# Optimization experiments

Measured on AMD Instinct MI355X. Metric: run time of the kernel, lower is better.

## Reference

```python
import jax, jax.numpy as jnp
import numpy as np
import itertools, math

DIM = 3          # Cl(3,0), Euclidean metric (1,1,1)
N_BLADES = 2 ** DIM   # 8
N_GRADES = DIM + 1    # 4 subspaces with sizes [1,3,3,1]
EPS = 1e-6

def _build_algebra():
    # blades ordered by grade then lexicographic, matching CEGNN's CliffordAlgebra
    blades = [()] + [c for g in range(1, DIM + 1) for c in itertools.combinations(range(DIM), g)]
    masks = [sum(1 << i for i in b) for b in blades]
    idx = {m: i for i, m in enumerate(masks)}
    grades = np.array([bin(m).count('1') for m in masks])

    def sign(a, b):  # reordering sign for e_A * e_B (Euclidean: squares are +1)
        s, aa = 0, a >> 1
        while aa:
            s += bin(aa & b).count('1')
            aa >>= 1
        return (-1.0) ** s

    cayley = np.zeros((N_BLADES, N_BLADES, N_BLADES), np.float32)
    for i, mi in enumerate(masks):
        for k, mk in enumerate(masks):
            cayley[i, idx[mi ^ mk], k] = sign(mi, mk)  # out_j = x_i C[i,j,k] y_k

    paths = np.zeros((N_GRADES, N_GRADES, N_GRADES), bool)
    for gi in range(N_GRADES):
        for gj in range(N_GRADES):
            for gk in range(N_GRADES):
                paths[gi, gj, gk] = np.any(cayley[np.ix_(grades == gi, grades == gj, grades == gk)] != 0)
    return cayley, grades, paths

CAYLEY, GRADES, PATHS = _build_algebra()
PATH_IDX = np.argwhere(PATHS)                                  # [20, 3]
GRADE_IDX = [np.nonzero(GRADES == g)[0] for g in range(N_GRADES)]
N_PATHS = int(PATHS.sum())                                     # 20 for Cl(3,0)

B, F = 8192, 256


def setup_inputs() -> dict:
    key = jax.random.key(0)
    ks = jax.random.split(key, 4)
    std_lin = 1.0 / math.sqrt(F)
    x = jax.random.normal(ks[0], (B, F, N_BLADES), jnp.float32)
    w_left = jax.random.normal(ks[1], (F, F, N_GRADES), jnp.float32) * std_lin
    b_left = jnp.zeros((1, F, 1), jnp.float32)
    w_right = jax.random.normal(ks[2], (F, F, N_GRADES), jnp.float32) * std_lin
    a_norm = jnp.zeros((F, N_GRADES), jnp.float32)
    w_gp = jax.random.normal(ks[3], (F, N_PATHS), jnp.float32) * (1.0 / math.sqrt(DIM + 1))
    return {"x": x, "w_left": w_left, "b_left": b_left, "w_right": w_right,
            "a_norm": a_norm, "w_gp": w_gp}


def _mv_linear(x, w):
    # w: [n, m, n_grades] -> repeat_interleave by grade sizes via gather to [n, m, 8]
    return jnp.einsum('bmi,nmi->bni', x, w[:, :, GRADES])


def _normalize(xr, a_norm):
    # per-grade smooth-abs-sqrt norm: (q^2 + 1e-16)^0.25, q = sum of squares (Euclidean)
    qs = jnp.stack([jnp.sum(xr[..., gi] ** 2, axis=-1) for gi in GRADE_IDX], axis=-1)  # [b,f,4]
    norms = (qs ** 2 + 1e-16) ** 0.25
    norms = jax.nn.sigmoid(a_norm) * (norms - 1.0) + 1.0
    return xr / (norms[..., GRADES] + EPS)


def reference(x, w_left, b_left, w_right, a_norm, w_gp):
    xr = _normalize(_mv_linear(x, w_right), a_norm)
    # scatter the 20 path weights into [F,4,4,4], expand grades to blades, mask by cayley
    wd = jnp.zeros((F, N_GRADES, N_GRADES, N_GRADES), x.dtype)
    wd = wd.at[:, PATH_IDX[:, 0], PATH_IDX[:, 1], PATH_IDX[:, 2]].set(w_gp)
    w = jnp.asarray(CAYLEY) * wd[:, GRADES][:, :, GRADES][:, :, :, GRADES]  # [F,8,8,8]
    gp = jnp.einsum('bni,nijk,bnk->bnj', x, w, xr)
    left = _mv_linear(x, w_left).at[..., 0].add(b_left[:, :, 0])  # bias embedded in scalar blade
    return (left + gp) / math.sqrt(2.0)
```

## Files before the change

### kernel.cpp

```cpp
#include <hip/hip_runtime.h>
#include <math.h>

namespace {

constexpr int Bsz = 8192;
constexpr int Fsz = 256;

struct Tables {
  int   jidx[64];
  float sgn[64];
  int   path[64];
  int   gr[8];
};

constexpr int cpopc(int v) { int c = 0; while (v) { c += v & 1; v >>= 1; } return c; }

constexpr Tables make_tables() {
  Tables t{};
  constexpr int MASKS[8] = {0, 1, 2, 4, 3, 5, 6, 7};
  int inv[8] = {};
  for (int i = 0; i < 8; ++i) inv[MASKS[i]] = i;
  int grade[8] = {};
  for (int i = 0; i < 8; ++i) { grade[i] = cpopc(MASKS[i]); t.gr[i] = grade[i]; }
  int pidx[4][4][4] = {};
  for (int a = 0; a < 4; ++a)
    for (int b = 0; b < 4; ++b)
      for (int c = 0; c < 4; ++c) pidx[a][b][c] = -1;
  int np = 0;
  for (int gi = 0; gi < 4; ++gi)
    for (int gj = 0; gj < 4; ++gj)
      for (int gk = 0; gk < 4; ++gk) {
        bool any = false;
        for (int i = 0; i < 8; ++i)
          for (int k = 0; k < 8; ++k)
            if (grade[i] == gi && grade[k] == gk && cpopc(MASKS[i] ^ MASKS[k]) == gj) any = true;
        if (any) pidx[gi][gj][gk] = np++;
      }
  for (int i = 0; i < 8; ++i)
    for (int k = 0; k < 8; ++k) {
      const int mi = MASKS[i], mk = MASKS[k];
      int s = 0, aa = mi >> 1;
      while (aa) { s += cpopc(aa & mk); aa >>= 1; }
      t.jidx[i * 8 + k] = inv[mi ^ mk];
      t.sgn[i * 8 + k]  = (s & 1) ? -1.0f : 1.0f;
      t.path[i * 8 + k] = pidx[grade[i]][cpopc(mi ^ mk)][grade[k]];
    }
  return t;
}

typedef __attribute__((ext_vector_type(8))) _Float16 f16x8;
typedef __attribute__((ext_vector_type(4))) float f32x4;

struct f8 { float v[8]; };

__device__ inline f8 ld8(const float* p) {
  f8 r;
  float4 a = *(const float4*)p;
  float4 b = *(const float4*)(p + 4);
  r.v[0] = a.x; r.v[1] = a.y; r.v[2] = a.z; r.v[3] = a.w;
  r.v[4] = b.x; r.v[5] = b.y; r.v[6] = b.z; r.v[7] = b.w;
  return r;
}

__device__ __forceinline__ unsigned short f2h(float f) {
  _Float16 h = (_Float16)f;
  return __builtin_bit_cast(unsigned short, h);
}

__global__ __launch_bounds__(256) void prep_all(
    const float* __restrict__ x, const float* __restrict__ wl,
    const float* __restrict__ wr,
    unsigned short* __restrict__ xhf, unsigned short* __restrict__ whf)
{
  const int blk = blockIdx.x;
  if (blk < 1024) {
    const int t = blk * 256 + threadIdx.x;
    const int b = t >> 5;
    const int m0 = (t & 31) << 3;
    const float* src = x + (((size_t)b << 8) + m0) * 8;
    float4 v[16];
    #pragma unroll
    for (int j = 0; j < 16; ++j) v[j] = ((const float4*)src)[j];
    const float* vf = (const float*)v;
    #pragma unroll
    for (int i = 0; i < 8; ++i) {
      unsigned int w0 = (unsigned int)f2h(vf[0 * 8 + i]) | ((unsigned int)f2h(vf[1 * 8 + i]) << 16);
      unsigned int w1 = (unsigned int)f2h(vf[2 * 8 + i]) | ((unsigned int)f2h(vf[3 * 8 + i]) << 16);
      unsigned int w2 = (unsigned int)f2h(vf[4 * 8 + i]) | ((unsigned int)f2h(vf[5 * 8 + i]) << 16);
      unsigned int w3 = (unsigned int)f2h(vf[6 * 8 + i]) | ((unsigned int)f2h(vf[7 * 8 + i]) << 16);
      const size_t o = ((size_t)i << 21) + ((size_t)b << 8) + m0;
      *(uint4*)(xhf + o) = make_uint4(w0, w1, w2, w3);
    }
  } else {
    const int t = (blk - 1024) * 256 + threadIdx.x;
    const int sg = t >> 14;
    const int s = sg >> 2, g = sg & 3;
    const int rem = t & 16383;
    const int n = rem >> 6;
    const int m0 = (rem & 63) << 2;
    const float* w = s ? wr : wl;
    ushort4 hv;
    hv.x = f2h(w[(((size_t)n << 8) + m0 + 0) * 4 + g]);
    hv.y = f2h(w[(((size_t)n << 8) + m0 + 1) * 4 + g]);
    hv.z = f2h(w[(((size_t)n << 8) + m0 + 2) * 4 + g]);
    hv.w = f2h(w[(((size_t)n << 8) + m0 + 3) * 4 + g]);
    const size_t o = ((size_t)sg << 16) + ((size_t)n << 8) + m0;
    *(ushort4*)(whf + o) = hv;
  }
}

struct KF { f16x8 Ah0, Ah1, Bh0, Bh1, Bh2, Bh3; };

struct Ptrs {
  const unsigned short *aH0, *aH1;
  const unsigned short *bH0, *bH1, *bH2, *bH3;
};

__device__ __forceinline__ void loadk(KF& f, const Ptrs& p, int ko) {
  f.Ah0 = *(const f16x8*)(p.aH0 + ko); f.Ah1 = *(const f16x8*)(p.aH1 + ko);
  f.Bh0 = *(const f16x8*)(p.bH0 + ko); f.Bh1 = *(const f16x8*)(p.bH1 + ko);
  f.Bh2 = *(const f16x8*)(p.bH2 + ko); f.Bh3 = *(const f16x8*)(p.bH3 + ko);
}

__device__ __forceinline__ void mfmak(const KF& f, f32x4 (&acc)[2][4]) {
#define MF1(NS, BH) \
  acc[0][NS] = __builtin_amdgcn_mfma_f32_16x16x32_f16(f.Ah0, f.BH, acc[0][NS], 0, 0, 0); \
  acc[1][NS] = __builtin_amdgcn_mfma_f32_16x16x32_f16(f.Ah1, f.BH, acc[1][NS], 0, 0, 0);
  MF1(0, Bh0)
  MF1(1, Bh1)
  MF1(2, Bh2)
  MF1(3, Bh3)
#undef MF1
}

#define SB() __builtin_amdgcn_sched_barrier(0)

constexpr int EXR = 545;

__global__ __launch_bounds__(512) void sgp_mfma(
    const float* __restrict__ x,
    const float* __restrict__ blft,
    const float* __restrict__ an,
    const float* __restrict__ wgp,
    const unsigned short* __restrict__ xhf,
    const unsigned short* __restrict__ whf,
    float* __restrict__ out)
{
  constexpr Tables T = make_tables();

  __shared__ __align__(16) float ex[16 * EXR];

  const int tid = threadIdx.x;
  const int wid = tid >> 6;
  const int lane = tid & 63;

  const int lin = blockIdx.x;
  const int xcd = lin & 7;
  const int j = lin >> 3;
  const int bt = (xcd << 5) | (j >> 3);
  const int nt = j & 7;
  const int bb = bt << 5;
  const int nn = nt << 5;

  const int gI = T.gr[wid];
  const int l15 = lane & 15;
  const int klane = (lane >> 4) << 3;

  Ptrs P;
  P.aH0 = xhf + ((size_t)wid << 21) + ((size_t)(bb + l15) << 8) + klane;
  P.aH1 = xhf + ((size_t)wid << 21) + ((size_t)(bb + 16 + l15) << 8) + klane;
  {
    const int pl0 = gI;
    const int pl1 = 4 + gI;
    const int r0 = nn + l15, r1 = nn + 16 + l15;
    P.bH0 = whf + ((size_t)pl0 << 16) + ((size_t)r0 << 8) + klane;
    P.bH1 = whf + ((size_t)pl0 << 16) + ((size_t)r1 << 8) + klane;
    P.bH2 = whf + ((size_t)pl1 << 16) + ((size_t)r0 << 8) + klane;
    P.bH3 = whf + ((size_t)pl1 << 16) + ((size_t)r1 << 8) + klane;
  }

  f32x4 acc[2][4];
  #pragma unroll
  for (int a = 0; a < 2; ++a)
    #pragma unroll
    for (int c = 0; c < 4; ++c) acc[a][c] = (f32x4)(0.0f);

  KF f0, f1, f2;
  loadk(f0, P, 0);    SB();
  loadk(f1, P, 32);   SB();
  loadk(f2, P, 64);   SB();
  mfmak(f0, acc);     SB();
  loadk(f0, P, 96);   SB();
  mfmak(f1, acc);     SB();
  loadk(f1, P, 128);  SB();
  mfmak(f2, acc);     SB();
  loadk(f2, P, 160);  SB();
  mfmak(f0, acc);     SB();
  loadk(f0, P, 192);  SB();
  mfmak(f1, acc);     SB();
  loadk(f1, P, 224);  SB();
  mfmak(f2, acc);     SB();
  mfmak(f0, acc);     SB();
  mfmak(f1, acc);

  const float inv_sqrt2 = 0.7071067811865476f;

  #pragma unroll
  for (int c = 0; c < 2; ++c) {
    if (c) __syncthreads();
    #pragma unroll
    for (int ns = 0; ns < 4; ++ns) {
      const int n = ((ns & 1) << 4) + l15;
      const int so = ((ns >> 1) << 3) + wid;
      #pragma unroll
      for (int r = 0; r < 4; ++r) {
        const int row = ((lane >> 4) << 2) + r;
        ex[row * EXR + n * 17 + so] = acc[c][ns][r];
      }
    }
    __syncthreads();

    const int prow = tid >> 5, pn = tid & 31;
    const float* e = &ex[prow * EXR + pn * 17];
    float L[8], R[8];
    #pragma unroll
    for (int i = 0; i < 8; ++i) { L[i] = e[i]; R[i] = e[8 + i]; }

    const int b  = bb + (c << 4) + prow;
    const int ng = nn + pn;

    float4 anv = *(const float4*)(an + (size_t)ng * 4);
    const float bias = blft[ng];
    float wd[20];
    #pragma unroll
    for (int q = 0; q < 5; ++q) {
      float4 w4 = *(const float4*)(wgp + (size_t)ng * 20 + q * 4);
      wd[q * 4 + 0] = w4.x; wd[q * 4 + 1] = w4.y;
      wd[q * 4 + 2] = w4.z; wd[q * 4 + 3] = w4.w;
    }
    float sgm[4];
    sgm[0] = 1.f / (1.f + expf(-anv.x));
    sgm[1] = 1.f / (1.f + expf(-anv.y));
    sgm[2] = 1.f / (1.f + expf(-anv.z));
    sgm[3] = 1.f / (1.f + expf(-anv.w));

    float q0 = R[0] * R[0];
    float q1 = R[1] * R[1] + R[2] * R[2] + R[3] * R[3];
    float q2 = R[4] * R[4] + R[5] * R[5] + R[6] * R[6];
    float q3 = R[7] * R[7];
    float nrm[4];
    nrm[0] = sqrtf(sqrtf(q0 * q0 + 1e-16f));
    nrm[1] = sqrtf(sqrtf(q1 * q1 + 1e-16f));
    nrm[2] = sqrtf(sqrtf(q2 * q2 + 1e-16f));
    nrm[3] = sqrtf(sqrtf(q3 * q3 + 1e-16f));
    float invn[4];
    #pragma unroll
    for (int g = 0; g < 4; ++g)
      invn[g] = 1.0f / (sgm[g] * (nrm[g] - 1.0f) + 1.0f + 1e-6f);

    float xr[8];
    #pragma unroll
    for (int i = 0; i < 8; ++i) xr[i] = R[i] * invn[T.gr[i]];

    f8 xv = ld8(x + (((size_t)b << 8) + ng) * 8);

    float gp[8] = {0, 0, 0, 0, 0, 0, 0, 0};
    #pragma unroll
    for (int i = 0; i < 8; ++i) {
      #pragma unroll
      for (int k = 0; k < 8; ++k) {
        const int p = i * 8 + k;
        gp[T.jidx[p]] += T.sgn[p] * wd[T.path[p]] * xv.v[i] * xr[k];
      }
    }

    float o[8];
    #pragma unroll
    for (int i = 0; i < 8; ++i)
      o[i] = (L[i] + gp[i] + (i == 0 ? bias : 0.f)) * inv_sqrt2;

    float4* dst = (float4*)(out + (((size_t)b << 8) + ng) * 8);
    dst[0] = make_float4(o[0], o[1], o[2], o[3]);
    dst[1] = make_float4(o[4], o[5], o[6], o[7]);
  }
}


constexpr int BT = 32;
constexpr int NT = 32;
constexpr int MT = 16;
constexpr int RS = 12;
constexpr int MS = BT * RS + 4;

__global__ __launch_bounds__(256) void sgp_fused(
    const float* __restrict__ x,
    const float* __restrict__ wl,
    const float* __restrict__ blft,
    const float* __restrict__ wr,
    const float* __restrict__ an,
    const float* __restrict__ wgp,
    float* __restrict__ out)
{
  constexpr Tables T = make_tables();

  __shared__ float xs[MT * MS];
  __shared__ float wsh[MT * MS];

  const int tid = threadIdx.x;
  const int tx = tid & 15;
  const int ty = tid >> 4;
  const int bb = blockIdx.x * BT;
  const int nn = blockIdx.y * NT;

  const int rl = tid >> 4;
  const int cm = tid & 15;

  float accL[2][2][8];
  float accR[2][2][8];
  #pragma unroll
  for (int a = 0; a < 2; ++a)
    #pragma unroll
    for (int c = 0; c < 2; ++c)
      #pragma unroll
      for (int i = 0; i < 8; ++i) { accL[a][c][i] = 0.f; accR[a][c][i] = 0.f; }

  for (int mm = 0; mm < Fsz; mm += MT) {
    {
      const float* g0 = x + (((size_t)(bb + rl)) * Fsz + (mm + cm)) * 8;
      const float* g1 = x + (((size_t)(bb + rl + 16)) * Fsz + (mm + cm)) * 8;
      float4 a0 = ((const float4*)g0)[0];
      float4 a1 = ((const float4*)g0)[1];
      float4 b0 = ((const float4*)g1)[0];
      float4 b1 = ((const float4*)g1)[1];
      *(float4*)&xs[cm * MS + rl * RS + 0] = a0;
      *(float4*)&xs[cm * MS + rl * RS + 4] = a1;
      *(float4*)&xs[cm * MS + (rl + 16) * RS + 0] = b0;
      *(float4*)&xs[cm * MS + (rl + 16) * RS + 4] = b1;
      float4 l0 = *(const float4*)(wl + (((size_t)(nn + rl)) * Fsz + (mm + cm)) * 4);
      float4 l1 = *(const float4*)(wl + (((size_t)(nn + rl + 16)) * Fsz + (mm + cm)) * 4);
      float4 r0 = *(const float4*)(wr + (((size_t)(nn + rl)) * Fsz + (mm + cm)) * 4);
      float4 r1 = *(const float4*)(wr + (((size_t)(nn + rl + 16)) * Fsz + (mm + cm)) * 4);
      *(float4*)&wsh[cm * MS + rl * RS + 0] = l0;
      *(float4*)&wsh[cm * MS + rl * RS + 4] = r0;
      *(float4*)&wsh[cm * MS + (rl + 16) * RS + 0] = l1;
      *(float4*)&wsh[cm * MS + (rl + 16) * RS + 4] = r1;
    }
    __syncthreads();

    #pragma unroll
    for (int m = 0; m < MT; ++m) {
      f8 xf0 = ld8(&xs[m * MS + ty * RS]);
      f8 xf1 = ld8(&xs[m * MS + (ty + 16) * RS]);
      f8 wv0 = ld8(&wsh[m * MS + tx * RS]);
      f8 wv1 = ld8(&wsh[m * MS + (tx + 16) * RS]);

      #pragma unroll
      for (int i = 0; i < 8; ++i) {
        const int g = T.gr[i];
        accL[0][0][i] += xf0.v[i] * wv0.v[g];
        accR[0][0][i] += xf0.v[i] * wv0.v[4 + g];
        accL[0][1][i] += xf0.v[i] * wv1.v[g];
        accR[0][1][i] += xf0.v[i] * wv1.v[4 + g];
        accL[1][0][i] += xf1.v[i] * wv0.v[g];
        accR[1][0][i] += xf1.v[i] * wv0.v[4 + g];
        accL[1][1][i] += xf1.v[i] * wv1.v[g];
        accR[1][1][i] += xf1.v[i] * wv1.v[4 + g];
      }
    }
    __syncthreads();
  }

  const float inv_sqrt2 = 0.7071067811865476f;

  #pragma unroll
  for (int c = 0; c < 2; ++c) {
    const int n = nn + tx + c * 16;
    float4 anv = *(const float4*)(an + (size_t)n * 4);
    const float bias = blft[n];
    float wd[20];
    #pragma unroll
    for (int q = 0; q < 5; ++q) {
      float4 w4 = *(const float4*)(wgp + (size_t)n * 20 + q * 4);
      wd[q * 4 + 0] = w4.x; wd[q * 4 + 1] = w4.y;
      wd[q * 4 + 2] = w4.z; wd[q * 4 + 3] = w4.w;
    }
    float sg[4];
    sg[0] = 1.f / (1.f + expf(-anv.x));
    sg[1] = 1.f / (1.f + expf(-anv.y));
    sg[2] = 1.f / (1.f + expf(-anv.z));
    sg[3] = 1.f / (1.f + expf(-anv.w));

    #pragma unroll
    for (int a = 0; a < 2; ++a) {
      const int b = bb + ty + a * 16;
      const float* r = accR[a][c];

      float q0 = r[0] * r[0];
      float q1 = r[1] * r[1] + r[2] * r[2] + r[3] * r[3];
      float q2 = r[4] * r[4] + r[5] * r[5] + r[6] * r[6];
      float q3 = r[7] * r[7];
      float nrm[4];
      nrm[0] = sqrtf(sqrtf(q0 * q0 + 1e-16f));
      nrm[1] = sqrtf(sqrtf(q1 * q1 + 1e-16f));
      nrm[2] = sqrtf(sqrtf(q2 * q2 + 1e-16f));
      nrm[3] = sqrtf(sqrtf(q3 * q3 + 1e-16f));
      float invn[4];
      #pragma unroll
      for (int g = 0; g < 4; ++g)
        invn[g] = 1.0f / (sg[g] * (nrm[g] - 1.0f) + 1.0f + 1e-6f);

      float xr[8];
      #pragma unroll
      for (int i = 0; i < 8; ++i) xr[i] = r[i] * invn[T.gr[i]];

      f8 xv = ld8(x + (((size_t)b) * Fsz + n) * 8);

      float gp[8] = {0, 0, 0, 0, 0, 0, 0, 0};
      #pragma unroll
      for (int i = 0; i < 8; ++i) {
        #pragma unroll
        for (int k = 0; k < 8; ++k) {
          const int p = i * 8 + k;
          gp[T.jidx[p]] += T.sgn[p] * wd[T.path[p]] * xv.v[i] * xr[k];
        }
      }

      float o[8];
      #pragma unroll
      for (int i = 0; i < 8; ++i)
        o[i] = (accL[a][c][i] + gp[i] + (i == 0 ? bias : 0.f)) * inv_sqrt2;

      float4* dst = (float4*)(out + (((size_t)b) * Fsz + n) * 8);
      dst[0] = make_float4(o[0], o[1], o[2], o[3]);
      dst[1] = make_float4(o[4], o[5], o[6], o[7]);
    }
  }
}

}

extern "C" void kernel_launch(void* const* d_in, const int* in_sizes, int n_in,
                              void* d_out, int out_size, void* d_ws, size_t ws_size,
                              hipStream_t stream) {
  const float* x   = (const float*)d_in[0];
  const float* wl  = (const float*)d_in[1];
  const float* bl  = (const float*)d_in[2];
  const float* wr  = (const float*)d_in[3];
  const float* an  = (const float*)d_in[4];
  const float* wgp = (const float*)d_in[5];
  float* out = (float*)d_out;

  const size_t NXE = (size_t)8 * Bsz * Fsz;
  const size_t NWE = (size_t)8 * Fsz * Fsz;
  const size_t need = (NXE + NWE) * sizeof(unsigned short);

  if (d_ws != nullptr && ws_size >= need) {
    unsigned short* xhf = (unsigned short*)d_ws;
    unsigned short* whf = xhf + NXE;

    prep_all<<<dim3(1536), dim3(256), 0, stream>>>(x, wl, wr, xhf, whf);
    sgp_mfma<<<dim3(2048), dim3(512), 0, stream>>>(
        x, bl, an, wgp, xhf, whf, out);
  } else {
    dim3 grid(Bsz / BT, Fsz / NT);
    sgp_fused<<<grid, dim3(256), 0, stream>>>(x, wl, bl, wr, an, wgp, out);
  }
}
```

Before: 246.6 us.

## Double batch tile per block to reuse weight fragments across more rows

Each block now covers 64 batch rows instead of 32, holding four A-row fragments and a 4x4 accumulator array, and the grid shrinks to 1024 blocks. Each loaded weight fragment is reused across twice as many MFMAs, cutting weight traffic per output. The epilogue loop runs four chunks through shared memory. The cost is higher register pressure from more accumulators and triple-buffered fragments, plus fewer blocks to hide latency.

```diff
diff --git a/kernel.cpp b/kernel.cpp
--- a/kernel.cpp
+++ b/kernel.cpp
@@ -109,28 +109,28 @@
   }
 }
 
-struct KF { f16x8 Ah0, Ah1, Bh0, Bh1, Bh2, Bh3; };
+constexpr int NBR = 4;
+
+struct KF { f16x8 A[NBR]; f16x8 B[4]; };
 
 struct Ptrs {
-  const unsigned short *aH0, *aH1;
-  const unsigned short *bH0, *bH1, *bH2, *bH3;
+  const unsigned short* a[NBR];
+  const unsigned short* b[4];
 };
 
 __device__ __forceinline__ void loadk(KF& f, const Ptrs& p, int ko) {
-  f.Ah0 = *(const f16x8*)(p.aH0 + ko); f.Ah1 = *(const f16x8*)(p.aH1 + ko);
-  f.Bh0 = *(const f16x8*)(p.bH0 + ko); f.Bh1 = *(const f16x8*)(p.bH1 + ko);
-  f.Bh2 = *(const f16x8*)(p.bH2 + ko); f.Bh3 = *(const f16x8*)(p.bH3 + ko);
-}
-
-__device__ __forceinline__ void mfmak(const KF& f, f32x4 (&acc)[2][4]) {
-#define MF1(NS, BH) \
-  acc[0][NS] = __builtin_amdgcn_mfma_f32_16x16x32_f16(f.Ah0, f.BH, acc[0][NS], 0, 0, 0); \
-  acc[1][NS] = __builtin_amdgcn_mfma_f32_16x16x32_f16(f.Ah1, f.BH, acc[1][NS], 0, 0, 0);
-  MF1(0, Bh0)
-  MF1(1, Bh1)
-  MF1(2, Bh2)
-  MF1(3, Bh3)
-#undef MF1
+  #pragma unroll
+  for (int r = 0; r < NBR; ++r) f.A[r] = *(const f16x8*)(p.a[r] + ko);
+  #pragma unroll
+  for (int n = 0; n < 4; ++n)  f.B[n] = *(const f16x8*)(p.b[n] + ko);
+}
+
+__device__ __forceinline__ void mfmak(const KF& f, f32x4 (&acc)[NBR][4]) {
+  #pragma unroll
+  for (int ns = 0; ns < 4; ++ns)
+    #pragma unroll
+    for (int r = 0; r < NBR; ++r)
+      acc[r][ns] = __builtin_amdgcn_mfma_f32_16x16x32_f16(f.A[r], f.B[ns], acc[r][ns], 0, 0, 0);
 }
 
 #define SB() __builtin_amdgcn_sched_barrier(0)
@@ -157,9 +157,9 @@
   const int lin = blockIdx.x;
   const int xcd = lin & 7;
   const int j = lin >> 3;
-  const int bt = (xcd << 5) | (j >> 3);
+  const int bt = (xcd << 4) | (j >> 3);
   const int nt = j & 7;
-  const int bb = bt << 5;
+  const int bb = bt << 6;
   const int nn = nt << 5;
 
   const int gI = T.gr[wid];
@@ -167,23 +167,21 @@
   const int klane = (lane >> 4) << 3;
 
   Ptrs P;
-  P.aH0 = xhf + ((size_t)wid << 21) + ((size_t)(bb + l15) << 8) + klane;
-  P.aH1 = xhf + ((size_t)wid << 21) + ((size_t)(bb + 16 + l15) << 8) + klane;
-  {
-    const int pl0 = gI;
-    const int pl1 = 4 + gI;
-    const int r0 = nn + l15, r1 = nn + 16 + l15;
-    P.bH0 = whf + ((size_t)pl0 << 16) + ((size_t)r0 << 8) + klane;
-    P.bH1 = whf + ((size_t)pl0 << 16) + ((size_t)r1 << 8) + klane;
-    P.bH2 = whf + ((size_t)pl1 << 16) + ((size_t)r0 << 8) + klane;
-    P.bH3 = whf + ((size_t)pl1 << 16) + ((size_t)r1 << 8) + klane;
-  }
-
-  f32x4 acc[2][4];
-  #pragma unroll
-  for (int a = 0; a < 2; ++a)
-    #pragma unroll
-    for (int c = 0; c < 4; ++c) acc[a][c] = (f32x4)(0.0f);
+  #pragma unroll
+  for (int r = 0; r < NBR; ++r)
+    P.a[r] = xhf + ((size_t)wid << 21) + ((size_t)(bb + (r << 4) + l15) << 8) + klane;
+  #pragma unroll
+  for (int ns = 0; ns < 4; ++ns) {
+    const int plane = ((ns >> 1) << 2) + gI;
+    P.b[ns] = whf + ((size_t)plane << 16)
+            + ((size_t)(nn + ((ns & 1) << 4) + l15) << 8) + klane;
+  }
+
+  f32x4 acc[NBR][4];
+  #pragma unroll
+  for (int r = 0; r < NBR; ++r)
+    #pragma unroll
+    for (int c = 0; c < 4; ++c) acc[r][c] = (f32x4)(0.0f);
 
   KF f0, f1, f2;
   loadk(f0, P, 0);    SB();
@@ -206,7 +204,7 @@
   const float inv_sqrt2 = 0.7071067811865476f;
 
   #pragma unroll
-  for (int c = 0; c < 2; ++c) {
+  for (int c = 0; c < NBR; ++c) {
     if (c) __syncthreads();
     #pragma unroll
     for (int ns = 0; ns < 4; ++ns) {
@@ -459,7 +457,7 @@
     unsigned short* whf = xhf + NXE;
 
     prep_all<<<dim3(1536), dim3(256), 0, stream>>>(x, wl, wr, xhf, whf);
-    sgp_mfma<<<dim3(2048), dim3(512), 0, stream>>>(
+    sgp_mfma<<<dim3(1024), dim3(512), 0, stream>>>(
         x, bl, an, wgp, xhf, whf, out);
   } else {
     dim3 grid(Bsz / BT, Fsz / NT);
```

Result: faster. 219.6 us (-11.0%).
